# Kernel optimization log

Hardware: AMD Instinct MI355X
Metric: run time of the kernel (lower is better)

The kernel has to match this reference:

```python
import jax, jax.numpy as jnp
import numpy as np

H = 8  # n_heads


def setup_inputs() -> dict:
    key = jax.random.key(0)
    ks = jax.random.split(key, 14)
    B, Lq, Lk, D = 8, 1024, 1024, 512  # batch, query len, kv len, in_dim
    d = 512                            # per-head out dim (out_dim before *= n_heads)
    s = 0.02                           # weight init scale
    x = jax.random.normal(ks[0], (B, Lq, D), jnp.float32)
    y = jax.random.normal(ks[1], (B, Lk, D), jnp.float32)
    x_pos = jax.random.normal(ks[2], (B, Lq, D), jnp.float32)
    y_pos = jax.random.normal(ks[3], (B, Lk, D), jnp.float32)
    x_mask = jnp.ones((B, Lq), dtype=bool)
    y_mask = jax.random.randint(ks[4], (B, Lk), 0, 2).astype(bool)
    Wq = jax.random.normal(ks[5], (H * d, D), jnp.float32) * s
    bq = jax.random.normal(ks[6], (H * d,), jnp.float32) * s
    Wk = jax.random.normal(ks[7], (H * d, D), jnp.float32) * s
    bk = jax.random.normal(ks[8], (H * d,), jnp.float32) * s
    Wv = jax.random.normal(ks[9], (H * d, D), jnp.float32) * s
    bv = jax.random.normal(ks[10], (H * d,), jnp.float32) * s
    Wp = jax.random.normal(ks[11], (d, D), jnp.float32) * s  # residual projection, no bias
    gamma = jax.random.uniform(ks[12], (H, 1, 1, 1), jnp.float32) + 0.001
    return dict(x=x, y=y, x_mask=x_mask, y_mask=y_mask, x_pos=x_pos, y_pos=y_pos,
                Wq=Wq, bq=bq, Wk=Wk, bk=bk, Wv=Wv, bv=bv, Wp=Wp, gamma=gamma)


def reference(x, y, x_mask, y_mask, x_pos, y_pos, Wq, bq, Wk, bk, Wv, bv, Wp, gamma):
    B, Lq, D = x.shape
    nH = gamma.shape[0]
    # QKV projections; query/key use positional-augmented inputs (with_pose)
    q = (x + x_pos) @ Wq.T + bq            # [B, Lq, H*d]
    k = (y + y_pos) @ Wk.T + bk            # [B, Lk, H*d]
    v = y @ Wv.T + bv                      # [B, Lk, H*d]
    d = q.shape[-1] // nH

    def heads(t):
        # split_cat: split last dim into H chunks, stack as leading head dim -> [H, B, L, d]
        return t.reshape(B, -1, nH, d).transpose(2, 0, 1, 3)

    qh, kh, vh = heads(q), heads(k), heads(v)
    # Unscaled attention energy (module applies no 1/sqrt(d) scaling)
    energy = jnp.einsum('hbqd,hbkd->hbqk', qh, kh)     # [H, B, Lq, Lk]
    mask = x_mask[:, :, None] & y_mask[:, None, :]     # [B, Lq, Lk]
    energy = jnp.where(mask[None], energy, -jnp.inf)
    attn = jax.nn.softmax(energy, axis=-1)
    out = jnp.einsum('hbqk,hbkd->hbqd', attn, vh)      # [H, B, Lq, d]
    # Gated residual: project x to per-head dim, blend with learnable gamma
    xp = x @ Wp.T                                      # [B, Lq, d]
    out = (gamma * out + xp[None]) / (gamma + 1.0)
    return out.transpose(1, 0, 2, 3)                   # [B, H, Lq, d]
```

## Files before the change

### kernel.cpp

```cpp
#include <hip/hip_runtime.h>


typedef __attribute__((ext_vector_type(8))) short short8;
typedef __attribute__((ext_vector_type(4))) float f32x4;
typedef __attribute__((ext_vector_type(4))) unsigned short ushort4v;

__device__ __forceinline__ unsigned short f2bf(float f) {
  unsigned int u = __builtin_bit_cast(unsigned int, f);
  u = (u + 0x7fffu + ((u >> 16) & 1u)) >> 16;
  return (unsigned short)u;
}

__device__ __forceinline__ f32x4 mfma16(short8 a, short8 b, f32x4 c) {
  return __builtin_amdgcn_mfma_f32_16x16x32_bf16(a, b, c, 0, 0, 0);
}

__device__ __forceinline__ void gld16(void* l, const void* g) {
  __builtin_amdgcn_global_load_lds(
      (const __attribute__((address_space(1))) unsigned int*)(unsigned long long)(__SIZE_TYPE__)g,
      (__attribute__((address_space(3))) unsigned int*)(unsigned int)(__SIZE_TYPE__)l,
      16, 0, 0);
}


__global__ void detect_mask_kernel(const void* __restrict__ ym, int* __restrict__ flag) {
  __shared__ int bad_i, bad_f;
  if (threadIdx.x == 0) { bad_i = 0; bad_f = 0; }
  __syncthreads();
  const int* ip = (const int*)ym;
  const float* fp = (const float*)ym;
  for (int i = threadIdx.x; i < 2048; i += 256) {
    int v = ip[i];
    if (v != 0 && v != 1) bad_i = 1;
    float f = fp[i];
    if (!(f == 0.0f || f == 1.0f)) bad_f = 1;
  }
  __syncthreads();
  if (threadIdx.x == 0) *flag = bad_i ? (bad_f ? 0 : 2) : 1;
}

__global__ __launch_bounds__(256) void conv_add2(const float* __restrict__ a,
                                                 const float* __restrict__ b,
                                                 unsigned short* __restrict__ o) {
  size_t base = ((size_t)blockIdx.x * 256 + threadIdx.x) * 8;
  f32x4 v0 = *(const f32x4*)(a + base), v1 = *(const f32x4*)(a + base + 4);
  f32x4 u0 = *(const f32x4*)(b + base), u1 = *(const f32x4*)(b + base + 4);
  v0 += u0; v1 += u1;
  short8 sv;
#pragma unroll
  for (int e = 0; e < 4; e++) { sv[e] = (short)f2bf(v0[e]); sv[4 + e] = (short)f2bf(v1[e]); }
  *(short8*)(o + base) = sv;
}

__global__ __launch_bounds__(256) void conv1(const float* __restrict__ a,
                                             unsigned short* __restrict__ o) {
  size_t base = ((size_t)blockIdx.x * 256 + threadIdx.x) * 8;
  f32x4 v0 = *(const f32x4*)(a + base), v1 = *(const f32x4*)(a + base + 4);
  short8 sv;
#pragma unroll
  for (int e = 0; e < 4; e++) { sv[e] = (short)f2bf(v0[e]); sv[4 + e] = (short)f2bf(v1[e]); }
  *(short8*)(o + base) = sv;
}

template<int STAGE, int BIASF, int MODE>
__global__ __launch_bounds__(256, 2) void gemm_k512(
    const void* __restrict__ Av, const void* __restrict__ Bv,
    const float* __restrict__ bias, void* __restrict__ out, int N)
{
  constexpr int K = 512;
  __shared__ unsigned short As[2][128][64];
  __shared__ unsigned short Bs[2][128][64];
  const int tid = threadIdx.x;
  const int w = tid >> 6, lane = tid & 63, g = lane >> 4, r16 = lane & 15;
  const int nwg = gridDim.x, flat = blockIdx.x;
  const int swz = (flat & 7) * (nwg >> 3) + (flat >> 3);
  const int m0 = (swz & 63) * 128, n0 = (swz >> 6) * 128;
  const int mblk = (w & 1) * 64, nblk = (w >> 1) * 64;

  auto stage = [&](int bb, int k0) {
    if (STAGE == 0) {
      const unsigned short* Ab = (const unsigned short*)Av;
      const unsigned short* Bb = (const unsigned short*)Bv;
#pragma unroll
      for (int i = 0; i < 4; i++) {
        int row0 = (w * 4 + i) * 8;
        int row = row0 + (lane >> 3), c = (lane & 7) ^ (row & 7);
        gld16(&As[bb][row0][0], Ab + (size_t)(m0 + row) * K + k0 + c * 8);
      }
#pragma unroll
      for (int i = 0; i < 4; i++) {
        int row0 = (w * 4 + i) * 8;
        int row = row0 + (lane >> 3), c = (lane & 7) ^ (row & 7);
        gld16(&Bs[bb][row0][0], Bb + (size_t)(n0 + row) * K + k0 + c * 8);
      }
    } else {
      const float* Af = (const float*)Av;
      const float* Bf = (const float*)Bv;
#pragma unroll
      for (int c = 0; c < 4; c++) {
        int fl = c * 256 + tid, row = fl >> 3, c8 = fl & 7;
        const float* px = Af + (size_t)(m0 + row) * K + k0 + c8 * 8;
        f32x4 v0 = *(const f32x4*)px, v1 = *(const f32x4*)(px + 4);
        short8 sv;
#pragma unroll
        for (int e = 0; e < 4; e++) { sv[e] = (short)f2bf(v0[e]); sv[4 + e] = (short)f2bf(v1[e]); }
        *(short8*)&As[bb][row][(c8 ^ (row & 7)) * 8] = sv;
      }
#pragma unroll
      for (int c = 0; c < 4; c++) {
        int fl = c * 256 + tid, row = fl >> 3, c8 = fl & 7;
        const float* pw = Bf + (size_t)(n0 + row) * K + k0 + c8 * 8;
        f32x4 v0 = *(const f32x4*)pw, v1 = *(const f32x4*)(pw + 4);
        short8 sv;
#pragma unroll
        for (int e = 0; e < 4; e++) { sv[e] = (short)f2bf(v0[e]); sv[4 + e] = (short)f2bf(v1[e]); }
        *(short8*)&Bs[bb][row][(c8 ^ (row & 7)) * 8] = sv;
      }
    }
  };

  f32x4 acc[4][4];
#pragma unroll
  for (int i = 0; i < 4; i++)
#pragma unroll
    for (int j = 0; j < 4; j++) acc[i][j] = f32x4{0.f, 0.f, 0.f, 0.f};

  stage(0, 0);
  __syncthreads();

  for (int t = 0; t < 8; t++) {
    const int cur = t & 1;
    if (t < 7) stage(cur ^ 1, (t + 1) * 64);
#pragma unroll
    for (int kk = 0; kk < 2; kk++) {
      short8 af[4], bfv[4];
#pragma unroll
      for (int mt = 0; mt < 4; mt++)
        af[mt] = *(const short8*)&As[cur][mblk + mt * 16 + r16][(((kk * 4 + g)) ^ (r16 & 7)) * 8];
#pragma unroll
      for (int nt = 0; nt < 4; nt++)
        bfv[nt] = *(const short8*)&Bs[cur][nblk + nt * 16 + r16][(((kk * 4 + g)) ^ (r16 & 7)) * 8];
#pragma unroll
      for (int mt = 0; mt < 4; mt++)
#pragma unroll
        for (int nt = 0; nt < 4; nt++)
          acc[mt][nt] = mfma16(af[mt], bfv[nt], acc[mt][nt]);
    }
    __syncthreads();
  }

#pragma unroll
  for (int nt = 0; nt < 4; nt++) {
    int n_g = n0 + nblk + nt * 16 + r16;
    float bval = BIASF ? bias[n_g] : 0.0f;
#pragma unroll
    for (int mt = 0; mt < 4; mt++) {
      int row4 = m0 + mblk + mt * 16 + g * 4;
      if (MODE == 1) {
        int bB = row4 >> 10, tok = row4 & 1023, hh = n_g >> 9, dh = n_g & 511;
        int t32 = tok & ~31, a = (tok & 31) >> 2;
        int ptok = t32 + ((a & 3) << 3) + ((a >> 2) << 2);
        ushort4v pk;
#pragma unroll
        for (int r = 0; r < 4; r++) pk[r] = f2bf(acc[mt][nt][r] + bval);
        *(ushort4v*)((unsigned short*)out + ((size_t)(bB * 8 + hh) * 512 + dh) * 1024 + ptok) = pk;
      } else if (MODE == 0) {
#pragma unroll
        for (int r = 0; r < 4; r++)
          ((unsigned short*)out)[(size_t)(row4 + r) * N + n_g] = f2bf(acc[mt][nt][r] + bval);
      } else {
#pragma unroll
        for (int r = 0; r < 4; r++)
          ((float*)out)[(size_t)(row4 + r) * N + n_g] = acc[mt][nt][r] + bval;
      }
    }
  }
}

__global__ __launch_bounds__(512, 2) void attn_kernel(
    const unsigned short* __restrict__ qptr, const unsigned short* __restrict__ kptr,
    const unsigned short* __restrict__ vtptr, const float* __restrict__ xpptr,
    const void* __restrict__ ymask, const int* __restrict__ mflag,
    const float* __restrict__ gamma, float* __restrict__ outp)
{
  __shared__ unsigned short Ks[2][32][512];
  __shared__ unsigned short Vs[2][512][32];
  __shared__ float mb[1024];

  int flat = blockIdx.y * 8 + blockIdx.x;
  int wg = (flat & 7) * 64 + (flat >> 3);
  int bh = wg >> 3, qt = wg & 7;
  int b = bh >> 3, h = bh & 7;
  int q0 = qt * 128;
  const int tid = threadIdx.x, w = tid >> 6, lane = tid & 63, g = lane >> 4, r16 = lane & 15;
  const int fm = *mflag;

  for (int i = tid; i < 1024; i += 512) {
    int keyg = b * 1024 + i;
    bool valid;
    if (fm == 1)      valid = ((const int*)ymask)[keyg] != 0;
    else if (fm == 2) valid = ((const float*)ymask)[keyg] != 0.0f;
    else              valid = ((const unsigned char*)ymask)[keyg] != 0;
    mb[i] = valid ? 0.0f : -2e30f;
  }

  const unsigned short* kbase = kptr + (size_t)(b * 1024) * 4096 + h * 512;
  const unsigned short* vbase = vtptr + (size_t)(bh * 512) * 1024;

  short8 qf[16];
  {
    const unsigned short* qrow = qptr + (size_t)(b * 1024 + q0 + w * 16 + r16) * 4096 + h * 512;
#pragma unroll
    for (int kk = 0; kk < 16; kk++) qf[kk] = *(const short8*)(qrow + kk * 32 + g * 8);
  }

  f32x4 o[32];
#pragma unroll
  for (int i = 0; i < 32; i++) o[i] = f32x4{0.f, 0.f, 0.f, 0.f};
  float m_run = -1e30f, l_run = 0.0f;

#pragma unroll
  for (int i = 0; i < 4; i++) {
    int r = w * 4 + i;
    gld16(&Ks[0][r][0], kbase + (size_t)r * 4096 + ((unsigned)(lane ^ (r & 7)) << 3));
  }
#pragma unroll
  for (int j = 0; j < 4; j++) {
    int dim0 = w * 64 + j * 16;
    gld16(&Vs[0][dim0][0], vbase + (size_t)(dim0 + (lane >> 2)) * 1024 + (lane & 3) * 8);
  }
  __syncthreads();

  for (int kt = 0; kt < 32; kt++) {
    const int cur = kt & 1, nxt = cur ^ 1;
    if (kt < 31) {
#pragma unroll
      for (int i = 0; i < 4; i++) {
        int r = w * 4 + i;
        gld16(&Ks[nxt][r][0],
              kbase + (size_t)((kt + 1) * 32 + r) * 4096 + ((unsigned)(lane ^ (r & 7)) << 3));
      }
#pragma unroll
      for (int j = 0; j < 4; j++) {
        int dim0 = w * 64 + j * 16;
        gld16(&Vs[nxt][dim0][0],
              vbase + (size_t)(dim0 + (lane >> 2)) * 1024 + (kt + 1) * 32 + (lane & 3) * 8);
      }
    }

    f32x4 s0a = f32x4{0.f,0.f,0.f,0.f}, s0b = f32x4{0.f,0.f,0.f,0.f};
    f32x4 s1a = f32x4{0.f,0.f,0.f,0.f}, s1b = f32x4{0.f,0.f,0.f,0.f};
    __builtin_amdgcn_s_setprio(1);
#pragma unroll
    for (int kk = 0; kk < 16; kk += 2) {
      short8 a0 = *(const short8*)&Ks[cur][r16][((kk * 4 + g) ^ (r16 & 7)) * 8];
      short8 a1 = *(const short8*)&Ks[cur][16 + r16][((kk * 4 + g) ^ (r16 & 7)) * 8];
      s0a = mfma16(a0, qf[kk], s0a);
      s1a = mfma16(a1, qf[kk], s1a);
      short8 c0 = *(const short8*)&Ks[cur][r16][(((kk + 1) * 4 + g) ^ (r16 & 7)) * 8];
      short8 c1 = *(const short8*)&Ks[cur][16 + r16][(((kk + 1) * 4 + g) ^ (r16 & 7)) * 8];
      s0b = mfma16(c0, qf[kk + 1], s0b);
      s1b = mfma16(c1, qf[kk + 1], s1b);
    }
    __builtin_amdgcn_s_setprio(0);
    f32x4 s0 = s0a + s0b, s1 = s1a + s1b;

    int kb = kt * 32 + 4 * g;
#pragma unroll
    for (int r = 0; r < 4; r++) { s0[r] += mb[kb + r]; s1[r] += mb[kb + 16 + r]; }

    float mx = fmaxf(fmaxf(fmaxf(s0[0], s0[1]), fmaxf(s0[2], s0[3])),
                     fmaxf(fmaxf(s1[0], s1[1]), fmaxf(s1[2], s1[3])));
    mx = fmaxf(mx, __shfl_xor(mx, 16));
    mx = fmaxf(mx, __shfl_xor(mx, 32));
    float mn = fmaxf(m_run, mx);
    float alpha = __expf(m_run - mn);
    m_run = mn;
    float p0[4], p1[4], sum = 0.0f;
#pragma unroll
    for (int r = 0; r < 4; r++) {
      p0[r] = (s0[r] < -1e29f) ? 0.0f : __expf(s0[r] - mn);
      p1[r] = (s1[r] < -1e29f) ? 0.0f : __expf(s1[r] - mn);
      sum += p0[r] + p1[r];
    }
    sum += __shfl_xor(sum, 16);
    sum += __shfl_xor(sum, 32);
    l_run = l_run * alpha + sum;

    if (!__all(alpha == 1.0f)) {
      float ao[4];
#pragma unroll
      for (int r = 0; r < 4; r++)
        ao[r] = __shfl(alpha, (lane & 48) | (4 * ((lane >> 4) & 3) + r));
#pragma unroll
      for (int nt = 0; nt < 32; nt++)
#pragma unroll
        for (int r = 0; r < 4; r++) o[nt][r] *= ao[r];
    }

    short8 pa;
#pragma unroll
    for (int e = 0; e < 4; e++) { pa[e] = (short)f2bf(p0[e]); pa[4 + e] = (short)f2bf(p1[e]); }

    __builtin_amdgcn_s_setprio(1);
#pragma unroll
    for (int nt = 0; nt < 32; nt++) {
      short8 bv = *(const short8*)&Vs[cur][nt * 16 + r16][g * 8];
      o[nt] = mfma16(pa, bv, o[nt]);
    }
    __builtin_amdgcn_s_setprio(0);
    __syncthreads();
  }

  float il[4];
#pragma unroll
  for (int r = 0; r < 4; r++)
    il[r] = 1.0f / __shfl(l_run, (lane & 48) | (4 * ((lane >> 4) & 3) + r));
  float gm = gamma[h];
  float c1 = gm / (gm + 1.0f), c2 = 1.0f / (gm + 1.0f);
#pragma unroll
  for (int nt = 0; nt < 32; nt++) {
    int dim = nt * 16 + r16;
#pragma unroll
    for (int r = 0; r < 4; r++) {
      int qrow = q0 + w * 16 + g * 4 + r;
      float xv = xpptr[(size_t)(b * 1024 + qrow) * 512 + dim];
      outp[((size_t)(b * 8 + h) * 1024 + qrow) * 512 + dim] = c1 * (o[nt][r] * il[r]) + c2 * xv;
    }
  }
}

extern "C" void kernel_launch(void* const* d_in, const int* in_sizes, int n_in,
                              void* d_out, int out_size, void* d_ws, size_t ws_size,
                              hipStream_t stream) {
  (void)in_sizes; (void)n_in; (void)out_size; (void)ws_size;
  const float* x     = (const float*)d_in[0];
  const float* y     = (const float*)d_in[1];
  const void*  ymask = d_in[3];
  const float* xpos  = (const float*)d_in[4];
  const float* ypos  = (const float*)d_in[5];
  const float* Wq    = (const float*)d_in[6];
  const float* bq    = (const float*)d_in[7];
  const float* Wk    = (const float*)d_in[8];
  const float* bk    = (const float*)d_in[9];
  const float* Wv    = (const float*)d_in[10];
  const float* bv    = (const float*)d_in[11];
  const float* Wp    = (const float*)d_in[12];
  const float* gamma = (const float*)d_in[13];

  char* ws = (char*)d_ws;
  unsigned short* q_ws  = (unsigned short*)(ws);
  unsigned short* k_ws  = (unsigned short*)(ws + (64ul << 20));
  unsigned short* xqb   = (unsigned short*)(ws + (64ul << 20));
  unsigned short* Wqb   = (unsigned short*)(ws + (72ul << 20));
  unsigned short* vt_ws = (unsigned short*)(ws + (128ul << 20));
  unsigned short* ykb   = (unsigned short*)(ws + (128ul << 20));
  unsigned short* Wkb   = (unsigned short*)(ws + (136ul << 20));
  unsigned short* xb    = (unsigned short*)(ws + (140ul << 20));
  unsigned short* Wpb   = (unsigned short*)(ws + (148ul << 20));
  float*          xp_ws = (float*)(ws + (192ul << 20));
  int*            flag  = (int*)(ws + (208ul << 20));

  detect_mask_kernel<<<1, 256, 0, stream>>>(ymask, flag);
  conv_add2<<<2048, 256, 0, stream>>>(x, xpos, xqb);
  conv1<<<1024, 256, 0, stream>>>(Wq, Wqb);
  conv_add2<<<2048, 256, 0, stream>>>(y, ypos, ykb);
  conv1<<<1024, 256, 0, stream>>>(Wk, Wkb);
  conv1<<<2048, 256, 0, stream>>>(x, xb);
  conv1<<<128, 256, 0, stream>>>(Wp, Wpb);

  gemm_k512<0, 1, 0><<<2048, 256, 0, stream>>>(xqb, Wqb, bq, q_ws, 4096);
  gemm_k512<0, 0, 2><<<256, 256, 0, stream>>>(xb, Wpb, nullptr, xp_ws, 512);
  gemm_k512<0, 1, 0><<<2048, 256, 0, stream>>>(ykb, Wkb, bk, k_ws, 4096);
  gemm_k512<1, 1, 1><<<2048, 256, 0, stream>>>(y, Wv, bv, vt_ws, 4096);

  attn_kernel<<<dim3(8, 64), 512, 0, stream>>>(q_ws, k_ws, vt_ws, xp_ws, ymask, flag,
                                               gamma, (float*)d_out);
}
```

Before: 574.5 us.

## Warp-specialize attention into score and PV wave groups with LDS P handoff

Splits the 8 waves of each attention block into 4 score waves (QK^T plus online softmax) and 4 output waves (P·V), which exchange bf16 probabilities and rescale factors through double-buffered shared memory. PV lags scores by one tile, and the query tile shrinks to 64 rows so twice as many blocks launch. The V staging gets a swizzle, and the masked-key guard on exp is removed. When the workspace is large enough, y and Wv are also pre-converted to bf16 before the V projection GEMM. This adds LDS traffic, an extra pipeline step, and halves per-block query reuse of K/V tiles.

Measured after the change: 811.1 us. 1.41x slower.

```diff
diff --git a/kernel.cpp b/kernel.cpp
--- a/kernel.cpp
+++ b/kernel.cpp
@@ -185,15 +185,20 @@
 {
   __shared__ unsigned short Ks[2][32][512];
   __shared__ unsigned short Vs[2][512][32];
+  __shared__ unsigned short Ps[2][64][32];
+  __shared__ float alph[2][64];
+  __shared__ float ilb[64];
   __shared__ float mb[1024];
 
-  int flat = blockIdx.y * 8 + blockIdx.x;
-  int wg = (flat & 7) * 64 + (flat >> 3);
-  int bh = wg >> 3, qt = wg & 7;
+  int flat = blockIdx.y * 16 + blockIdx.x;
+  int wg = (flat & 7) * 128 + (flat >> 3);
+  int bh = wg >> 4, qt4 = wg & 15;
   int b = bh >> 3, h = bh & 7;
-  int q0 = qt * 128;
+  int q0 = qt4 * 64;
   const int tid = threadIdx.x, w = tid >> 6, lane = tid & 63, g = lane >> 4, r16 = lane & 15;
   const int fm = *mflag;
+  const bool isS = (w < 4);
+  const int w4 = w & 3;
 
   for (int i = tid; i < 1024; i += 512) {
     int keyg = b * 1024 + i;
@@ -205,18 +210,20 @@
   }
 
   const unsigned short* kbase = kptr + (size_t)(b * 1024) * 4096 + h * 512;
-  const unsigned short* vbase = vtptr + (size_t)(bh * 512) * 1024;
+  const unsigned short* vbase = vtptr + (size_t)bh * 512 * 1024;
 
   short8 qf[16];
-  {
-    const unsigned short* qrow = qptr + (size_t)(b * 1024 + q0 + w * 16 + r16) * 4096 + h * 512;
+  if (isS) {
+    const unsigned short* qrow = qptr + (size_t)(b * 1024 + q0 + w4 * 16 + r16) * 4096 + h * 512;
 #pragma unroll
     for (int kk = 0; kk < 16; kk++) qf[kk] = *(const short8*)(qrow + kk * 32 + g * 8);
   }
 
-  f32x4 o[32];
-#pragma unroll
-  for (int i = 0; i < 32; i++) o[i] = f32x4{0.f, 0.f, 0.f, 0.f};
+  f32x4 o[4][8];
+#pragma unroll
+  for (int i = 0; i < 4; i++)
+#pragma unroll
+    for (int j = 0; j < 8; j++) o[i][j] = f32x4{0.f, 0.f, 0.f, 0.f};
   float m_run = -1e30f, l_run = 0.0f;
 
 #pragma unroll
@@ -224,108 +231,130 @@
     int r = w * 4 + i;
     gld16(&Ks[0][r][0], kbase + (size_t)r * 4096 + ((unsigned)(lane ^ (r & 7)) << 3));
   }
-#pragma unroll
-  for (int j = 0; j < 4; j++) {
-    int dim0 = w * 64 + j * 16;
-    gld16(&Vs[0][dim0][0], vbase + (size_t)(dim0 + (lane >> 2)) * 1024 + (lane & 3) * 8);
-  }
   __syncthreads();
 
-  for (int kt = 0; kt < 32; kt++) {
-    const int cur = kt & 1, nxt = cur ^ 1;
-    if (kt < 31) {
+  for (int t = 0; t <= 32; t++) {
+    const int cb = t & 1, pb = cb ^ 1;
+
+    if (t < 31) {
 #pragma unroll
       for (int i = 0; i < 4; i++) {
         int r = w * 4 + i;
-        gld16(&Ks[nxt][r][0],
-              kbase + (size_t)((kt + 1) * 32 + r) * 4096 + ((unsigned)(lane ^ (r & 7)) << 3));
-      }
+        gld16(&Ks[pb][r][0],
+              kbase + (size_t)((t + 1) * 32 + r) * 4096 + ((unsigned)(lane ^ (r & 7)) << 3));
+      }
+    }
+    if (t < 32) {
 #pragma unroll
       for (int j = 0; j < 4; j++) {
         int dim0 = w * 64 + j * 16;
-        gld16(&Vs[nxt][dim0][0],
-              vbase + (size_t)(dim0 + (lane >> 2)) * 1024 + (kt + 1) * 32 + (lane & 3) * 8);
-      }
-    }
-
-    f32x4 s0a = f32x4{0.f,0.f,0.f,0.f}, s0b = f32x4{0.f,0.f,0.f,0.f};
-    f32x4 s1a = f32x4{0.f,0.f,0.f,0.f}, s1b = f32x4{0.f,0.f,0.f,0.f};
-    __builtin_amdgcn_s_setprio(1);
-#pragma unroll
-    for (int kk = 0; kk < 16; kk += 2) {
-      short8 a0 = *(const short8*)&Ks[cur][r16][((kk * 4 + g) ^ (r16 & 7)) * 8];
-      short8 a1 = *(const short8*)&Ks[cur][16 + r16][((kk * 4 + g) ^ (r16 & 7)) * 8];
-      s0a = mfma16(a0, qf[kk], s0a);
-      s1a = mfma16(a1, qf[kk], s1a);
-      short8 c0 = *(const short8*)&Ks[cur][r16][(((kk + 1) * 4 + g) ^ (r16 & 7)) * 8];
-      short8 c1 = *(const short8*)&Ks[cur][16 + r16][(((kk + 1) * 4 + g) ^ (r16 & 7)) * 8];
-      s0b = mfma16(c0, qf[kk + 1], s0b);
-      s1b = mfma16(c1, qf[kk + 1], s1b);
-    }
-    __builtin_amdgcn_s_setprio(0);
-    f32x4 s0 = s0a + s0b, s1 = s1a + s1b;
-
-    int kb = kt * 32 + 4 * g;
-#pragma unroll
-    for (int r = 0; r < 4; r++) { s0[r] += mb[kb + r]; s1[r] += mb[kb + 16 + r]; }
-
-    float mx = fmaxf(fmaxf(fmaxf(s0[0], s0[1]), fmaxf(s0[2], s0[3])),
-                     fmaxf(fmaxf(s1[0], s1[1]), fmaxf(s1[2], s1[3])));
-    mx = fmaxf(mx, __shfl_xor(mx, 16));
-    mx = fmaxf(mx, __shfl_xor(mx, 32));
-    float mn = fmaxf(m_run, mx);
-    float alpha = __expf(m_run - mn);
-    m_run = mn;
-    float p0[4], p1[4], sum = 0.0f;
-#pragma unroll
-    for (int r = 0; r < 4; r++) {
-      p0[r] = (s0[r] < -1e29f) ? 0.0f : __expf(s0[r] - mn);
-      p1[r] = (s1[r] < -1e29f) ? 0.0f : __expf(s1[r] - mn);
-      sum += p0[r] + p1[r];
-    }
-    sum += __shfl_xor(sum, 16);
-    sum += __shfl_xor(sum, 32);
-    l_run = l_run * alpha + sum;
-
-    if (!__all(alpha == 1.0f)) {
-      float ao[4];
-#pragma unroll
-      for (int r = 0; r < 4; r++)
-        ao[r] = __shfl(alpha, (lane & 48) | (4 * ((lane >> 4) & 3) + r));
-#pragma unroll
-      for (int nt = 0; nt < 32; nt++)
-#pragma unroll
-        for (int r = 0; r < 4; r++) o[nt][r] *= ao[r];
-    }
-
-    short8 pa;
-#pragma unroll
-    for (int e = 0; e < 4; e++) { pa[e] = (short)f2bf(p0[e]); pa[4 + e] = (short)f2bf(p1[e]); }
-
-    __builtin_amdgcn_s_setprio(1);
-#pragma unroll
-    for (int nt = 0; nt < 32; nt++) {
-      short8 bv = *(const short8*)&Vs[cur][nt * 16 + r16][g * 8];
-      o[nt] = mfma16(pa, bv, o[nt]);
-    }
-    __builtin_amdgcn_s_setprio(0);
+        int drow = dim0 + (lane >> 2);
+        int p = (lane & 3) ^ ((drow >> 1) & 3);
+        gld16(&Vs[cb][dim0][0], vbase + (size_t)drow * 1024 + t * 32 + p * 8);
+      }
+    }
+
+    if (isS) {
+      if (t < 32) {
+        f32x4 s0a = f32x4{0.f,0.f,0.f,0.f}, s0b = f32x4{0.f,0.f,0.f,0.f};
+        f32x4 s1a = f32x4{0.f,0.f,0.f,0.f}, s1b = f32x4{0.f,0.f,0.f,0.f};
+        __builtin_amdgcn_s_setprio(1);
+#pragma unroll
+        for (int kk = 0; kk < 16; kk += 2) {
+          short8 a0 = *(const short8*)&Ks[cb][r16][((kk * 4 + g) ^ (r16 & 7)) * 8];
+          short8 a1 = *(const short8*)&Ks[cb][16 + r16][((kk * 4 + g) ^ (r16 & 7)) * 8];
+          s0a = mfma16(a0, qf[kk], s0a);
+          s1a = mfma16(a1, qf[kk], s1a);
+          short8 c0 = *(const short8*)&Ks[cb][r16][(((kk + 1) * 4 + g) ^ (r16 & 7)) * 8];
+          short8 c1 = *(const short8*)&Ks[cb][16 + r16][(((kk + 1) * 4 + g) ^ (r16 & 7)) * 8];
+          s0b = mfma16(c0, qf[kk + 1], s0b);
+          s1b = mfma16(c1, qf[kk + 1], s1b);
+        }
+        __builtin_amdgcn_s_setprio(0);
+        f32x4 s0 = s0a + s0b, s1 = s1a + s1b;
+
+        int kb = t * 32 + 4 * g;
+#pragma unroll
+        for (int r = 0; r < 4; r++) { s0[r] += mb[kb + r]; s1[r] += mb[kb + 16 + r]; }
+
+        float mx = fmaxf(fmaxf(fmaxf(s0[0], s0[1]), fmaxf(s0[2], s0[3])),
+                         fmaxf(fmaxf(s1[0], s1[1]), fmaxf(s1[2], s1[3])));
+        mx = fmaxf(mx, __shfl_xor(mx, 16));
+        mx = fmaxf(mx, __shfl_xor(mx, 32));
+        float mn = fmaxf(m_run, mx);
+        float alpha = __expf(m_run - mn);
+        m_run = mn;
+        float p0[4], p1[4], sum = 0.0f;
+#pragma unroll
+        for (int r = 0; r < 4; r++) {
+          p0[r] = __expf(s0[r] - mn);
+          p1[r] = __expf(s1[r] - mn);
+          sum += p0[r] + p1[r];
+        }
+        sum += __shfl_xor(sum, 16);
+        sum += __shfl_xor(sum, 32);
+        l_run = l_run * alpha + sum;
+
+        if (g == 0) alph[cb][w4 * 16 + r16] = alpha;
+        short8 pa;
+#pragma unroll
+        for (int e = 0; e < 4; e++) { pa[e] = (short)f2bf(p0[e]); pa[4 + e] = (short)f2bf(p1[e]); }
+        *(short8*)&Ps[cb][w4 * 16 + r16][(g ^ (r16 & 3)) * 8] = pa;
+      }
+    } else {
+      if (t >= 1) {
+        f32x4 af[4];
+#pragma unroll
+        for (int qt = 0; qt < 4; qt++) af[qt] = *(const f32x4*)&alph[pb][qt * 16 + g * 4];
+#pragma unroll
+        for (int qt = 0; qt < 4; qt++)
+#pragma unroll
+          for (int dt = 0; dt < 8; dt++)
+#pragma unroll
+            for (int r = 0; r < 4; r++) o[qt][dt][r] *= af[qt][r];
+
+        short8 paf[4], bvf[8];
+#pragma unroll
+        for (int qt = 0; qt < 4; qt++)
+          paf[qt] = *(const short8*)&Ps[pb][qt * 16 + r16][(g ^ (r16 & 3)) * 8];
+#pragma unroll
+        for (int dt = 0; dt < 8; dt++) {
+          int row = w4 * 128 + dt * 16 + r16;
+          bvf[dt] = *(const short8*)&Vs[pb][row][(g ^ ((row >> 1) & 3)) * 8];
+        }
+        __builtin_amdgcn_s_setprio(1);
+#pragma unroll
+        for (int qt = 0; qt < 4; qt++)
+#pragma unroll
+          for (int dt = 0; dt < 8; dt++)
+            o[qt][dt] = mfma16(paf[qt], bvf[dt], o[qt][dt]);
+        __builtin_amdgcn_s_setprio(0);
+      }
+    }
     __syncthreads();
   }
 
-  float il[4];
-#pragma unroll
-  for (int r = 0; r < 4; r++)
-    il[r] = 1.0f / __shfl(l_run, (lane & 48) | (4 * ((lane >> 4) & 3) + r));
-  float gm = gamma[h];
-  float c1 = gm / (gm + 1.0f), c2 = 1.0f / (gm + 1.0f);
-#pragma unroll
-  for (int nt = 0; nt < 32; nt++) {
-    int dim = nt * 16 + r16;
-#pragma unroll
-    for (int r = 0; r < 4; r++) {
-      int qrow = q0 + w * 16 + g * 4 + r;
-      float xv = xpptr[(size_t)(b * 1024 + qrow) * 512 + dim];
-      outp[((size_t)(b * 8 + h) * 1024 + qrow) * 512 + dim] = c1 * (o[nt][r] * il[r]) + c2 * xv;
+  if (isS) {
+    if (g == 0) ilb[w4 * 16 + r16] = 1.0f / l_run;
+  }
+  __syncthreads();
+  if (!isS) {
+    float gm = gamma[h];
+    float c1 = gm / (gm + 1.0f), c2 = 1.0f / (gm + 1.0f);
+#pragma unroll
+    for (int qt = 0; qt < 4; qt++) {
+      f32x4 iv = *(const f32x4*)&ilb[qt * 16 + g * 4];
+#pragma unroll
+      for (int dt = 0; dt < 8; dt++) {
+        int dim = w4 * 128 + dt * 16 + r16;
+#pragma unroll
+        for (int r = 0; r < 4; r++) {
+          int qrow = q0 + qt * 16 + g * 4 + r;
+          float xv = xpptr[(size_t)(b * 1024 + qrow) * 512 + dim];
+          outp[((size_t)(b * 8 + h) * 1024 + qrow) * 512 + dim] =
+              c1 * (o[qt][dt][r] * iv[r]) + c2 * xv;
+        }
+      }
     }
   }
 }
@@ -333,7 +362,7 @@
 extern "C" void kernel_launch(void* const* d_in, const int* in_sizes, int n_in,
                               void* d_out, int out_size, void* d_ws, size_t ws_size,
                               hipStream_t stream) {
-  (void)in_sizes; (void)n_in; (void)out_size; (void)ws_size;
+  (void)in_sizes; (void)n_in; (void)out_size;
   const float* x     = (const float*)d_in[0];
   const float* y     = (const float*)d_in[1];
   const void*  ymask = d_in[3];
@@ -360,6 +389,9 @@
   unsigned short* Wpb   = (unsigned short*)(ws + (148ul << 20));
   float*          xp_ws = (float*)(ws + (192ul << 20));
   int*            flag  = (int*)(ws + (208ul << 20));
+  unsigned short* yb    = (unsigned short*)(ws + (209ul << 20));
+  unsigned short* Wvb   = (unsigned short*)(ws + (217ul << 20));
+  const bool big = ws_size >= (221ul << 20);
 
   detect_mask_kernel<<<1, 256, 0, stream>>>(ymask, flag);
   conv_add2<<<2048, 256, 0, stream>>>(x, xpos, xqb);
@@ -368,12 +400,19 @@
   conv1<<<1024, 256, 0, stream>>>(Wk, Wkb);
   conv1<<<2048, 256, 0, stream>>>(x, xb);
   conv1<<<128, 256, 0, stream>>>(Wp, Wpb);
+  if (big) {
+    conv1<<<2048, 256, 0, stream>>>(y, yb);
+    conv1<<<1024, 256, 0, stream>>>(Wv, Wvb);
+  }
 
   gemm_k512<0, 1, 0><<<2048, 256, 0, stream>>>(xqb, Wqb, bq, q_ws, 4096);
   gemm_k512<0, 0, 2><<<256, 256, 0, stream>>>(xb, Wpb, nullptr, xp_ws, 512);
   gemm_k512<0, 1, 0><<<2048, 256, 0, stream>>>(ykb, Wkb, bk, k_ws, 4096);
-  gemm_k512<1, 1, 1><<<2048, 256, 0, stream>>>(y, Wv, bv, vt_ws, 4096);
-
-  attn_kernel<<<dim3(8, 64), 512, 0, stream>>>(q_ws, k_ws, vt_ws, xp_ws, ymask, flag,
-                                               gamma, (float*)d_out);
-}
+  if (big)
+    gemm_k512<0, 1, 1><<<2048, 256, 0, stream>>>(yb, Wvb, bv, vt_ws, 4096);
+  else
+    gemm_k512<1, 1, 1><<<2048, 256, 0, stream>>>(y, Wv, bv, vt_ws, 4096);
+
+  attn_kernel<<<dim3(16, 64), 512, 0, stream>>>(q_ws, k_ws, vt_ws, xp_ws, ymask, flag,
+                                                gamma, (float*)d_out);
+}
```
